# Kernel optimization log

Measured on AMD Instinct MI355X. Metric: run time of the kernel, lower is better.

## Reference

```python
import jax, jax.numpy as jnp
import numpy as np

B, S, D, H = 2, 2048, 2048, 16
DH = D // H
FF = 4 * D
EPS = 1e-5


def setup_inputs() -> dict:
    key = jax.random.key(0)
    ks = jax.random.split(key, 8)
    sd = 0.02
    return {
        "hidden_states": jax.random.normal(ks[0], (B, S, D), jnp.float32),
        "ln1_w": jnp.ones((D,), jnp.float32),
        "ln1_b": jnp.zeros((D,), jnp.float32),
        "qkv_w": jax.random.normal(ks[1], (3 * D, D), jnp.float32) * sd,
        "qkv_b": jnp.zeros((3 * D,), jnp.float32),
        "dense_w": jax.random.normal(ks[2], (D, D), jnp.float32) * sd,
        "dense_b": jnp.zeros((D,), jnp.float32),
        "ln2_w": jnp.ones((D,), jnp.float32),
        "ln2_b": jnp.zeros((D,), jnp.float32),
        "fc1_w": jax.random.normal(ks[3], (FF, D), jnp.float32) * sd,
        "fc1_b": jnp.zeros((FF,), jnp.float32),
        "fc2_w": jax.random.normal(ks[4], (D, FF), jnp.float32) * sd,
        "fc2_b": jnp.zeros((D,), jnp.float32),
    }


def _layer_norm(x, w, b):
    mu = jnp.mean(x, axis=-1, keepdims=True)
    var = jnp.mean(jnp.square(x - mu), axis=-1, keepdims=True)
    return (x - mu) * jax.lax.rsqrt(var + EPS) * w + b


def _attention(x, qkv_w, qkv_b, dense_w, dense_b):
    qkv = x @ qkv_w.T + qkv_b  # [B,S,3D]
    q, k, v = jnp.split(qkv, 3, axis=-1)
    q = q.reshape(B, S, H, DH)
    k = k.reshape(B, S, H, DH)
    v = v.reshape(B, S, H, DH)
    scale = DH ** -0.5
    scores = jnp.einsum("bqhd,bkhd->bhqk", q, k) * scale
    causal = jnp.tril(jnp.ones((S, S), bool))
    scores = jnp.where(causal, scores, jnp.finfo(scores.dtype).min)
    probs = jax.nn.softmax(scores, axis=-1)
    out = jnp.einsum("bhqk,bkhd->bqhd", probs, v).reshape(B, S, D)
    return out @ dense_w.T + dense_b


def reference(hidden_states, ln1_w, ln1_b, qkv_w, qkv_b, dense_w, dense_b,
              ln2_w, ln2_b, fc1_w, fc1_b, fc2_w, fc2_b):
    residual = hidden_states
    x = _layer_norm(hidden_states, ln1_w, ln1_b)
    x = _attention(x, qkv_w, qkv_b, dense_w, dense_b) + residual
    residual = x
    h = _layer_norm(x, ln2_w, ln2_b)
    h = jax.nn.gelu(h @ fc1_w.T + fc1_b, approximate=False)
    h = h @ fc2_w.T + fc2_b
    return residual + h
```

## Files before the change

kernel.cpp:

```cpp
#include <hip/hip_runtime.h>
#include <hip/hip_bf16.h>

#define SEQ    2048
#define DMODEL 2048
#define NHEAD  16
#define DHEAD  128
#define TOK    4096
#define TD     6144
#define FFDIM  8192

typedef __attribute__((ext_vector_type(4)))  float f32x4;
typedef __attribute__((ext_vector_type(16))) float f32x16;
typedef __attribute__((ext_vector_type(8)))  short short8v;

__device__ __forceinline__ void async_ld16(const void* src, void* lds) {
  __builtin_amdgcn_global_load_lds((const __attribute__((address_space(1))) void*)src,
                                   (__attribute__((address_space(3))) void*)lds, 16, 0, 0);
}

__device__ __forceinline__ unsigned pk2(float a, float b) {
  union { __hip_bfloat16 h[2]; unsigned u; } p;
  p.h[0] = __float2bfloat16(a);
  p.h[1] = __float2bfloat16(b);
  return p.u;
}

__global__ __launch_bounds__(256) void f2bf_kernel(const float* __restrict__ in,
                                                   __hip_bfloat16* __restrict__ out, long n) {
  long i0 = ((long)blockIdx.x * 256 + threadIdx.x) * 8;
  long stride = (long)gridDim.x * 256 * 8;
  for (long i = i0; i < n; i += stride) {
    float4 a = *(const float4*)(in + i);
    float4 b = *(const float4*)(in + i + 4);
    union { __hip_bfloat16 h[8]; int4 v; } p;
    p.h[0] = __float2bfloat16(a.x); p.h[1] = __float2bfloat16(a.y);
    p.h[2] = __float2bfloat16(a.z); p.h[3] = __float2bfloat16(a.w);
    p.h[4] = __float2bfloat16(b.x); p.h[5] = __float2bfloat16(b.y);
    p.h[6] = __float2bfloat16(b.z); p.h[7] = __float2bfloat16(b.w);
    *(int4*)(out + i) = p.v;
  }
}

__global__ __launch_bounds__(256) void ln_kernel(const float* __restrict__ x,
                                                 const float* __restrict__ w,
                                                 const float* __restrict__ b,
                                                 __hip_bfloat16* __restrict__ out) {
  __shared__ float red[8];
  const int row = blockIdx.x;
  const int tid = threadIdx.x;
  const float* xr = x + (long)row * DMODEL;
  float4 v0 = ((const float4*)xr)[tid * 2];
  float4 v1 = ((const float4*)xr)[tid * 2 + 1];
  float s  = v0.x + v0.y + v0.z + v0.w + v1.x + v1.y + v1.z + v1.w;
  float ss = v0.x*v0.x + v0.y*v0.y + v0.z*v0.z + v0.w*v0.w
           + v1.x*v1.x + v1.y*v1.y + v1.z*v1.z + v1.w*v1.w;
  #pragma unroll
  for (int m = 1; m < 64; m <<= 1) { s += __shfl_xor(s, m, 64); ss += __shfl_xor(ss, m, 64); }
  if ((tid & 63) == 0) { red[tid >> 6] = s; red[4 + (tid >> 6)] = ss; }
  __syncthreads();
  s  = red[0] + red[1] + red[2] + red[3];
  ss = red[4] + red[5] + red[6] + red[7];
  const float mu = s * (1.0f / DMODEL);
  const float rs = rsqrtf(ss * (1.0f / DMODEL) - mu * mu + 1e-5f);
  float4 w0 = ((const float4*)w)[tid * 2], w1 = ((const float4*)w)[tid * 2 + 1];
  float4 b0 = ((const float4*)b)[tid * 2], b1 = ((const float4*)b)[tid * 2 + 1];
  union { __hip_bfloat16 h[8]; int4 v; } p;
  p.h[0] = __float2bfloat16((v0.x - mu) * rs * w0.x + b0.x);
  p.h[1] = __float2bfloat16((v0.y - mu) * rs * w0.y + b0.y);
  p.h[2] = __float2bfloat16((v0.z - mu) * rs * w0.z + b0.z);
  p.h[3] = __float2bfloat16((v0.w - mu) * rs * w0.w + b0.w);
  p.h[4] = __float2bfloat16((v1.x - mu) * rs * w1.x + b1.x);
  p.h[5] = __float2bfloat16((v1.y - mu) * rs * w1.y + b1.y);
  p.h[6] = __float2bfloat16((v1.z - mu) * rs * w1.z + b1.z);
  p.h[7] = __float2bfloat16((v1.w - mu) * rs * w1.w + b1.w);
  ((int4*)(out + (long)row * DMODEL))[tid] = p.v;
}

template <int MODE, int BM>
__global__ __launch_bounds__(512, 2) void gemm8p(const __hip_bfloat16* __restrict__ A,
                                                 const __hip_bfloat16* __restrict__ B,
                                                 const float* __restrict__ bias,
                                                 const float* __restrict__ resid,
                                                 void* __restrict__ outp,
                                                 int N, long K) {
  constexpr int MR     = BM / 32;
  constexpr int MH     = MR / 2;
  constexpr int A_ISS  = BM / 128;
  constexpr int ABYTES = BM * 64;
  constexpr int BUFB   = ABYTES + 16384;
  __shared__ __align__(16) char lds[4 * BUFB];

  const int tid  = threadIdx.x;
  const int lane = tid & 63;
  const int w    = tid >> 6;
  const int wr   = w >> 2, wc = w & 3;
  const long m0  = (long)blockIdx.y * BM;
  const long n0  = (long)blockIdx.x * 256;
  const int  NT  = (int)(K >> 5);

  const int srow = w * 16 + (lane >> 2);
  const int schk = lane & 3;

  auto stageA = [&](int t) {
    char* base = lds + (t & 3) * BUFB;
    #pragma unroll
    for (int i = 0; i < A_ISS; ++i) {
      int row = srow + i * 128;
      long gc = (long)t * 32 + (long)((schk ^ (row & 3)) * 8);
      async_ld16(A + (m0 + row) * K + gc, base + i * 8192 + w * 1024);
    }
  };
  auto stageB = [&](int t) {
    char* base = lds + (t & 3) * BUFB + ABYTES;
    #pragma unroll
    for (int i = 0; i < 2; ++i) {
      int row = srow + i * 128;
      long gc = (long)t * 32 + (long)((schk ^ (row & 3)) * 8);
      async_ld16(B + (n0 + row) * K + gc, base + i * 8192 + w * 1024);
    }
  };

  f32x4 acc[MR][4] = {};

  #pragma unroll
  for (int t = 0; t < 4; ++t) { stageA(t); stageB(t); }
  if constexpr (BM == 256) asm volatile("s_waitcnt vmcnt(8)\ns_barrier" ::: "memory");
  else                     asm volatile("s_waitcnt vmcnt(6)\ns_barrier" ::: "memory");

  const int c16 = lane >> 4;
  const int l15 = lane & 15;

  for (int t = 0; t < NT; ++t) {
    const int st = (t + 3 < NT) ? t + 3 : NT - 1;
    const char* bb = lds + (t & 3) * BUFB;

    stageA(st);
    short8v bfr[4], af[MH];
    #pragma unroll
    for (int n = 0; n < 4; ++n) {
      int row = wc * 64 + n * 16 + l15;
      bfr[n] = *(const short8v*)(bb + ABYTES + row * 64 + ((c16 ^ (row & 3)) << 4));
    }
    #pragma unroll
    for (int m = 0; m < MH; ++m) {
      int row = wr * (BM / 2) + m * 16 + l15;
      af[m] = *(const short8v*)(bb + row * 64 + ((c16 ^ (row & 3)) << 4));
    }
    __builtin_amdgcn_s_setprio(1);
    #pragma unroll
    for (int m = 0; m < MH; ++m)
      #pragma unroll
      for (int n = 0; n < 4; ++n)
        acc[m][n] = __builtin_amdgcn_mfma_f32_16x16x32_bf16(af[m], bfr[n], acc[m][n], 0, 0, 0);
    __builtin_amdgcn_s_setprio(0);

    stageB(st);
    #pragma unroll
    for (int m = 0; m < MH; ++m) {
      int row = wr * (BM / 2) + (MH + m) * 16 + l15;
      af[m] = *(const short8v*)(bb + row * 64 + ((c16 ^ (row & 3)) << 4));
    }
    __builtin_amdgcn_s_setprio(1);
    #pragma unroll
    for (int m = 0; m < MH; ++m)
      #pragma unroll
      for (int n = 0; n < 4; ++n)
        acc[MH + m][n] = __builtin_amdgcn_mfma_f32_16x16x32_bf16(af[m], bfr[n], acc[MH + m][n], 0, 0, 0);
    __builtin_amdgcn_s_setprio(0);

    if constexpr (BM == 256) asm volatile("s_waitcnt vmcnt(8)\ns_barrier" ::: "memory");
    else                     asm volatile("s_waitcnt vmcnt(6)\ns_barrier" ::: "memory");
  }

  const int colq = l15;
  const int rowq = (lane >> 4) * 4;
  #pragma unroll
  for (int n = 0; n < 4; ++n) {
    long col = n0 + wc * 64 + n * 16 + colq;
    float bi = bias[col];
    #pragma unroll
    for (int mi = 0; mi < MR; ++mi) {
      long row0 = m0 + wr * (BM / 2) + mi * 16 + rowq;
      #pragma unroll
      for (int j = 0; j < 4; ++j) {
        long idx = (row0 + j) * (long)N + col;
        float v = acc[mi][n][j] + bi;
        if (MODE == 0) {
          ((__hip_bfloat16*)outp)[idx] = __float2bfloat16(v);
        } else if (MODE == 1) {
          ((float*)outp)[idx] = v + resid[idx];
        } else {
          float g = 0.5f * v * (1.0f + erff(v * 0.70710678118654752f));
          ((__hip_bfloat16*)outp)[idx] = __float2bfloat16(g);
        }
      }
    }
  }
}

#define QBLK 128
#define KVB  64
#define VSTR 144
#define KBYT 16384
#define VBYT (DHEAD * VSTR)
__global__ __launch_bounds__(256, 2) void attn_kernel(const __hip_bfloat16* __restrict__ qkv,
                                                      __hip_bfloat16* __restrict__ out) {
  __shared__ __align__(16) char smem[2 * KBYT + 2 * VBYT];
  const int tid = threadIdx.x, lane = tid & 63, wid = tid >> 6;
  const int l31 = lane & 31, hi = lane >> 5;
  const int qb = (int)gridDim.x - 1 - (int)blockIdx.x;
  const int q0 = qb * QBLK;
  const int bh = blockIdx.y;
  const int bb = bh >> 4, h = bh & 15;
  const long rowbase = (long)bb * SEQ;
  const int qcol = h * DHEAD, kcol = DMODEL + h * DHEAD, vcol = 2 * DMODEL + h * DHEAD;
  const int qw0 = q0 + wid * 32;

  short8v qf[8];
  {
    const __hip_bfloat16* qp = qkv + (rowbase + qw0 + l31) * TD + qcol + hi * 8;
    #pragma unroll
    for (int kc = 0; kc < 8; ++kc) qf[kc] = *(const short8v*)(qp + kc * 16);
  }

  f32x16 o[4] = {};
  float m_ = -1e30f, l_ = 0.0f;

  const int nt = (q0 + QBLK) / KVB;

  const int kv0s = (tid >> 4) * 4;
  const int dh0s = (tid & 15) * 8;
  auto k_stage = [&](int t) {
    char* kb = smem + (t & 1) * KBYT;
    const long kvr = rowbase + (long)t * KVB;
    #pragma unroll
    for (int i = 0; i < 4; ++i) {
      int c = i * 256 + tid;
      int row = c >> 4, slot = c & 15;
      const void* src = qkv + (kvr + row) * TD + kcol + ((slot ^ (row & 7)) << 3);
      async_ld16(src, kb + i * 4096 + wid * 1024);
    }
  };
  auto v_load = [&](int t, int4* r) {
    const long kvr = rowbase + (long)t * KVB;
    #pragma unroll
    for (int i = 0; i < 4; ++i)
      r[i] = *(const int4*)(qkv + (kvr + kv0s + i) * TD + vcol + dh0s);
  };
  auto v_write = [&](int t, const int4* r) {
    char* vt = smem + 2 * KBYT + (t & 1) * VBYT;
    union { int4 v; unsigned short s[8]; } u0, u1, u2, u3;
    u0.v = r[0]; u1.v = r[1]; u2.v = r[2]; u3.v = r[3];
    #pragma unroll
    for (int dd = 0; dd < 8; ++dd) {
      int d = (dd + ((tid >> 1) & 7)) & 7;
      unsigned lo = (unsigned)u0.s[d] | ((unsigned)u1.s[d] << 16);
      unsigned hi2 = (unsigned)u2.s[d] | ((unsigned)u3.s[d] << 16);
      uint2 wv; wv.x = lo; wv.y = hi2;
      *(uint2*)(vt + (dh0s + d) * VSTR + kv0s * 2) = wv;
    }
  };

  {
    int4 vr[4];
    v_load(0, vr);
    k_stage(0);
    v_write(0, vr);
  }
  __syncthreads();

  for (int t = 0; t < nt; ++t) {
    int4 vr[4];
    const bool more = (t + 1 < nt);
    if (more) { v_load(t + 1, vr); k_stage(t + 1); }

    const int kv0 = t * KVB;
    if (kv0 <= qw0 + 31) {
      const char* Kb = smem + (t & 1) * KBYT;
      f32x16 s0 = {}, s1 = {};
      #pragma unroll
      for (int kc = 0; kc < 8; ++kc) {
        const int colb = kc * 32 + hi * 16;
        const int r0 = l31, r1 = 32 + l31;
        short8v k0 = *(const short8v*)(Kb + r0 * 256 + (colb ^ ((r0 & 7) << 4)));
        short8v k1 = *(const short8v*)(Kb + r1 * 256 + (colb ^ ((r0 & 7) << 4)));
        s0 = __builtin_amdgcn_mfma_f32_32x32x16_bf16(k0, qf[kc], s0, 0, 0, 0);
        s1 = __builtin_amdgcn_mfma_f32_32x32x16_bf16(k1, qf[kc], s1, 0, 0, 0);
      }
      const float scale = 0.08838834764831845f;
      float sv[32];
      #pragma unroll
      for (int r = 0; r < 16; ++r) { sv[r] = s0[r] * scale; sv[16 + r] = s1[r] * scale; }
      const int qg = qw0 + l31;
      if (kv0 + KVB - 1 > qw0) {
        #pragma unroll
        for (int r = 0; r < 16; ++r) {
          int kvr_ = kv0 + (r & 3) + 8 * (r >> 2) + 4 * hi;
          if (kvr_ > qg)      sv[r]      = -1e30f;
          if (kvr_ + 32 > qg) sv[16 + r] = -1e30f;
        }
      }
      float pmax = sv[0];
      #pragma unroll
      for (int r = 1; r < 32; ++r) pmax = fmaxf(pmax, sv[r]);
      pmax = fmaxf(pmax, __shfl_xor(pmax, 32, 64));
      float mn = fmaxf(m_, pmax);
      float alpha = __expf(m_ - mn);
      m_ = mn;
      l_ *= alpha;
      #pragma unroll
      for (int d = 0; d < 4; ++d)
        #pragma unroll
        for (int r = 0; r < 16; ++r) o[d][r] *= alpha;
      float rsum = 0.0f;
      #pragma unroll
      for (int r = 0; r < 32; ++r) { sv[r] = __expf(sv[r] - m_); rsum += sv[r]; }
      l_ += rsum + __shfl_xor(rsum, 32, 64);
      int pa_[4][4];
      #pragma unroll
      for (int kc = 0; kc < 4; ++kc) {
        int ba = 16 * (kc >> 1) + 8 * (kc & 1);
        unsigned wA0 = pk2(sv[ba + 0], sv[ba + 1]);
        unsigned wA1 = pk2(sv[ba + 2], sv[ba + 3]);
        unsigned wB0 = pk2(sv[ba + 4], sv[ba + 5]);
        unsigned wB1 = pk2(sv[ba + 6], sv[ba + 7]);
        unsigned z0 = (unsigned)__shfl_xor((int)(hi ? wA0 : wB0), 32, 64);
        unsigned z1 = (unsigned)__shfl_xor((int)(hi ? wA1 : wB1), 32, 64);
        pa_[kc][0] = hi ? (int)z0 : (int)wA0;
        pa_[kc][1] = hi ? (int)z1 : (int)wA1;
        pa_[kc][2] = hi ? (int)wB0 : (int)z0;
        pa_[kc][3] = hi ? (int)wB1 : (int)z1;
      }
      const char* Vt = smem + 2 * KBYT + (t & 1) * VBYT;
      #pragma unroll
      for (int dht = 0; dht < 4; ++dht) {
        const int dh = dht * 32 + l31;
        short8v vf[4];
        #pragma unroll
        for (int kc = 0; kc < 4; ++kc)
          vf[kc] = *(const short8v*)(Vt + dh * VSTR + kc * 32 + hi * 16);
        #pragma unroll
        for (int kc = 0; kc < 4; ++kc) {
          union { int i[4]; short8v v; } bv;
          bv.i[0] = pa_[kc][0]; bv.i[1] = pa_[kc][1];
          bv.i[2] = pa_[kc][2]; bv.i[3] = pa_[kc][3];
          o[dht] = __builtin_amdgcn_mfma_f32_32x32x16_bf16(vf[kc], bv.v, o[dht], 0, 0, 0);
        }
      }
    }
    if (more) v_write(t + 1, vr);
    __syncthreads();
  }

  const float linv = 1.0f / l_;
  const long orow = (rowbase + qw0 + l31) * DMODEL + h * DHEAD;
  #pragma unroll
  for (int dht = 0; dht < 4; ++dht)
    #pragma unroll
    for (int rg = 0; rg < 4; ++rg) {
      union { __hip_bfloat16 hh[4]; uint2 u; } pk;
      #pragma unroll
      for (int i = 0; i < 4; ++i) pk.hh[i] = __float2bfloat16(o[dht][rg * 4 + i] * linv);
      *(uint2*)(out + orow + dht * 32 + 8 * rg + 4 * hi) = pk.u;
    }
}

extern "C" void kernel_launch(void* const* d_in, const int* in_sizes, int n_in,
                              void* d_out, int out_size, void* d_ws, size_t ws_size,
                              hipStream_t stream) {
  const float* hidden  = (const float*)d_in[0];
  const float* ln1w    = (const float*)d_in[1];
  const float* ln1b    = (const float*)d_in[2];
  const float* qkvw    = (const float*)d_in[3];
  const float* qkvb    = (const float*)d_in[4];
  const float* densew  = (const float*)d_in[5];
  const float* denseb  = (const float*)d_in[6];
  const float* ln2w    = (const float*)d_in[7];
  const float* ln2b    = (const float*)d_in[8];
  const float* fc1w    = (const float*)d_in[9];
  const float* fc1b    = (const float*)d_in[10];
  const float* fc2w    = (const float*)d_in[11];
  const float* fc2b    = (const float*)d_in[12];

  char* ws = (char*)d_ws;
  size_t off = 0;
  auto alloc = [&](size_t bytes) { char* p = ws + off; off += (bytes + 255) & ~(size_t)255; return p; };
  __hip_bfloat16* xbf    = (__hip_bfloat16*)alloc((size_t)TOK * DMODEL * 2);
  __hip_bfloat16* wqkv   = (__hip_bfloat16*)alloc((size_t)TD * DMODEL * 2);
  __hip_bfloat16* wdense = (__hip_bfloat16*)alloc((size_t)DMODEL * DMODEL * 2);
  __hip_bfloat16* wfc1   = (__hip_bfloat16*)alloc((size_t)FFDIM * DMODEL * 2);
  __hip_bfloat16* wfc2   = (__hip_bfloat16*)alloc((size_t)DMODEL * FFDIM * 2);
  __hip_bfloat16* big    = (__hip_bfloat16*)alloc((size_t)TOK * FFDIM * 2);
  float*          x2     = (float*)alloc((size_t)TOK * DMODEL * 4);
  __hip_bfloat16* qkvbuf  = big;
  __hip_bfloat16* attnout = big + (size_t)TOK * TD;
  __hip_bfloat16* gelubuf = big;

  f2bf_kernel<<<1024, 256, 0, stream>>>(qkvw,   wqkv,   (long)TD * DMODEL);
  f2bf_kernel<<<1024, 256, 0, stream>>>(densew, wdense, (long)DMODEL * DMODEL);
  f2bf_kernel<<<1024, 256, 0, stream>>>(fc1w,   wfc1,   (long)FFDIM * DMODEL);
  f2bf_kernel<<<1024, 256, 0, stream>>>(fc2w,   wfc2,   (long)DMODEL * FFDIM);

  ln_kernel<<<TOK, 256, 0, stream>>>(hidden, ln1w, ln1b, xbf);
  gemm8p<0, 256><<<dim3(TD / 256, TOK / 256), 512, 0, stream>>>(xbf, wqkv, qkvb, nullptr, qkvbuf, TD, DMODEL);
  attn_kernel<<<dim3(SEQ / QBLK, 2 * NHEAD), 256, 0, stream>>>(qkvbuf, attnout);
  gemm8p<1, 128><<<dim3(DMODEL / 256, TOK / 128), 512, 0, stream>>>(attnout, wdense, denseb, hidden, x2, DMODEL, DMODEL);
  ln_kernel<<<TOK, 256, 0, stream>>>(x2, ln2w, ln2b, xbf);
  gemm8p<2, 256><<<dim3(FFDIM / 256, TOK / 256), 512, 0, stream>>>(xbf, wfc1, fc1b, nullptr, gelubuf, FFDIM, DMODEL);
  gemm8p<1, 128><<<dim3(DMODEL / 256, TOK / 128), 512, 0, stream>>>(gelubuf, wfc2, fc2b, x2, (float*)d_out, DMODEL, FFDIM);
}
```

Before: 744.0 us.

## Replace pipelined GEMM with simple 128x128 tiled GEMM and pair attention query blocks

Swaps the four-stage async-pipelined 256-wide GEMM for a single-buffered 128x128 tile GEMM with 256 threads, 64-wide K steps, an XOR-swizzled LDS layout and an XCD-aware block swizzle. The attention kernel now processes two query blocks per workgroup (one from each end of the causal range) to balance work under the causal mask, halving the grid. The GEMM loses software pipelining and the larger-tile reuse, so loads and MFMA work are no longer overlapped within a block.

```diff
diff --git a/kernel.cpp b/kernel.cpp
--- a/kernel.cpp
+++ b/kernel.cpp
@@ -76,115 +76,81 @@
   ((int4*)(out + (long)row * DMODEL))[tid] = p.v;
 }
 
-template <int MODE, int BM>
-__global__ __launch_bounds__(512, 2) void gemm8p(const __hip_bfloat16* __restrict__ A,
-                                                 const __hip_bfloat16* __restrict__ B,
-                                                 const float* __restrict__ bias,
-                                                 const float* __restrict__ resid,
-                                                 void* __restrict__ outp,
-                                                 int N, long K) {
-  constexpr int MR     = BM / 32;
-  constexpr int MH     = MR / 2;
-  constexpr int A_ISS  = BM / 128;
-  constexpr int ABYTES = BM * 64;
-  constexpr int BUFB   = ABYTES + 16384;
-  __shared__ __align__(16) char lds[4 * BUFB];
-
-  const int tid  = threadIdx.x;
+template <int MODE>
+__global__ __launch_bounds__(256) void gemm_bt(const __hip_bfloat16* __restrict__ A,
+                                               const __hip_bfloat16* __restrict__ B,
+                                               const float* __restrict__ bias,
+                                               const float* __restrict__ resid,
+                                               void* __restrict__ outp,
+                                               int N, long K) {
+  __shared__ __align__(16) char lds[32768];
+  const int tid = threadIdx.x;
   const int lane = tid & 63;
-  const int w    = tid >> 6;
-  const int wr   = w >> 2, wc = w & 3;
-  const long m0  = (long)blockIdx.y * BM;
-  const long n0  = (long)blockIdx.x * 256;
-  const int  NT  = (int)(K >> 5);
-
-  const int srow = w * 16 + (lane >> 2);
-  const int schk = lane & 3;
-
-  auto stageA = [&](int t) {
-    char* base = lds + (t & 3) * BUFB;
-    #pragma unroll
-    for (int i = 0; i < A_ISS; ++i) {
-      int row = srow + i * 128;
-      long gc = (long)t * 32 + (long)((schk ^ (row & 3)) * 8);
-      async_ld16(A + (m0 + row) * K + gc, base + i * 8192 + w * 1024);
-    }
-  };
-  auto stageB = [&](int t) {
-    char* base = lds + (t & 3) * BUFB + ABYTES;
-    #pragma unroll
-    for (int i = 0; i < 2; ++i) {
-      int row = srow + i * 128;
-      long gc = (long)t * 32 + (long)((schk ^ (row & 3)) * 8);
-      async_ld16(B + (n0 + row) * K + gc, base + i * 8192 + w * 1024);
-    }
-  };
-
-  f32x4 acc[MR][4] = {};
-
-  #pragma unroll
-  for (int t = 0; t < 4; ++t) { stageA(t); stageB(t); }
-  if constexpr (BM == 256) asm volatile("s_waitcnt vmcnt(8)\ns_barrier" ::: "memory");
-  else                     asm volatile("s_waitcnt vmcnt(6)\ns_barrier" ::: "memory");
-
-  const int c16 = lane >> 4;
-  const int l15 = lane & 15;
-
-  for (int t = 0; t < NT; ++t) {
-    const int st = (t + 3 < NT) ? t + 3 : NT - 1;
-    const char* bb = lds + (t & 3) * BUFB;
-
-    stageA(st);
-    short8v bfr[4], af[MH];
-    #pragma unroll
-    for (int n = 0; n < 4; ++n) {
-      int row = wc * 64 + n * 16 + l15;
-      bfr[n] = *(const short8v*)(bb + ABYTES + row * 64 + ((c16 ^ (row & 3)) << 4));
-    }
-    #pragma unroll
-    for (int m = 0; m < MH; ++m) {
-      int row = wr * (BM / 2) + m * 16 + l15;
-      af[m] = *(const short8v*)(bb + row * 64 + ((c16 ^ (row & 3)) << 4));
-    }
-    __builtin_amdgcn_s_setprio(1);
-    #pragma unroll
-    for (int m = 0; m < MH; ++m)
-      #pragma unroll
-      for (int n = 0; n < 4; ++n)
-        acc[m][n] = __builtin_amdgcn_mfma_f32_16x16x32_bf16(af[m], bfr[n], acc[m][n], 0, 0, 0);
-    __builtin_amdgcn_s_setprio(0);
-
-    stageB(st);
-    #pragma unroll
-    for (int m = 0; m < MH; ++m) {
-      int row = wr * (BM / 2) + (MH + m) * 16 + l15;
-      af[m] = *(const short8v*)(bb + row * 64 + ((c16 ^ (row & 3)) << 4));
-    }
-    __builtin_amdgcn_s_setprio(1);
-    #pragma unroll
-    for (int m = 0; m < MH; ++m)
-      #pragma unroll
-      for (int n = 0; n < 4; ++n)
-        acc[MH + m][n] = __builtin_amdgcn_mfma_f32_16x16x32_bf16(af[m], bfr[n], acc[MH + m][n], 0, 0, 0);
-    __builtin_amdgcn_s_setprio(0);
-
-    if constexpr (BM == 256) asm volatile("s_waitcnt vmcnt(8)\ns_barrier" ::: "memory");
-    else                     asm volatile("s_waitcnt vmcnt(6)\ns_barrier" ::: "memory");
+  const int wid = tid >> 6;
+  const int wr = wid >> 1, wc = wid & 1;
+  const int gx = gridDim.x;
+  const int nwg = gx * (int)gridDim.y;
+  const int lin = (int)blockIdx.y * gx + (int)blockIdx.x;
+  const int cpx = nwg >> 3;
+  const int swz = (lin & 7) * cpx + (lin >> 3);
+  const long m0 = (long)(swz / gx) * 128;
+  const long n0 = (long)(swz % gx) * 128;
+
+  const int lrow = lane >> 3;
+  const long ksrc = (long)(((lane & 7) ^ lrow) * 8);
+
+  f32x4 acc[4][4] = {};
+
+  for (long kt = 0; kt < K; kt += 64) {
+    __syncthreads();
+    #pragma unroll
+    for (int c = 0; c < 8; ++c) {
+      int region = wid * 8 + c;
+      int isB = region >> 4;
+      int rr = region & 15;
+      int row = rr * 8 + lrow;
+      const __hip_bfloat16* srcbase = isB ? B : A;
+      long grow = (isB ? n0 : m0) + row;
+      const __hip_bfloat16* src = srcbase + grow * K + kt + ksrc;
+      async_ld16(src, lds + isB * 16384 + rr * 1024);
+    }
+    __syncthreads();
+    #pragma unroll
+    for (int kk = 0; kk < 2; ++kk) {
+      short8v af[4], bfr[4];
+      #pragma unroll
+      for (int m = 0; m < 4; ++m) {
+        int row = wr * 64 + m * 16 + (lane & 15);
+        int kb = kk * 64 + (lane >> 4) * 16;
+        af[m] = *(const short8v*)(lds + row * 128 + (kb ^ ((row & 7) << 4)));
+      }
+      #pragma unroll
+      for (int n = 0; n < 4; ++n) {
+        int row = wc * 64 + n * 16 + (lane & 15);
+        int kb = kk * 64 + (lane >> 4) * 16;
+        bfr[n] = *(const short8v*)(lds + 16384 + row * 128 + (kb ^ ((row & 7) << 4)));
+      }
+      #pragma unroll
+      for (int m = 0; m < 4; ++m)
+        #pragma unroll
+        for (int n = 0; n < 4; ++n)
+          acc[m][n] = __builtin_amdgcn_mfma_f32_16x16x32_bf16(af[m], bfr[n], acc[m][n], 0, 0, 0);
+    }
   }
 
-  const int colq = l15;
+  const int colq = lane & 15;
   const int rowq = (lane >> 4) * 4;
   #pragma unroll
   for (int n = 0; n < 4; ++n) {
     long col = n0 + wc * 64 + n * 16 + colq;
     float bi = bias[col];
     #pragma unroll
-    for (int mi = 0; mi < MR; ++mi) {
-      long row0 = m0 + wr * (BM / 2) + mi * 16 + rowq;
+    for (int m = 0; m < 4; ++m) {
+      long row0 = m0 + wr * 64 + m * 16 + rowq;
       #pragma unroll
       for (int j = 0; j < 4; ++j) {
         long idx = (row0 + j) * (long)N + col;
-        float v = acc[mi][n][j] + bi;
+        float v = acc[m][n][j] + bi;
         if (MODE == 0) {
           ((__hip_bfloat16*)outp)[idx] = __float2bfloat16(v);
         } else if (MODE == 1) {
@@ -208,25 +174,11 @@
   __shared__ __align__(16) char smem[2 * KBYT + 2 * VBYT];
   const int tid = threadIdx.x, lane = tid & 63, wid = tid >> 6;
   const int l31 = lane & 31, hi = lane >> 5;
-  const int qb = (int)gridDim.x - 1 - (int)blockIdx.x;
-  const int q0 = qb * QBLK;
+  const int bx = blockIdx.x;
   const int bh = blockIdx.y;
   const int bb = bh >> 4, h = bh & 15;
   const long rowbase = (long)bb * SEQ;
   const int qcol = h * DHEAD, kcol = DMODEL + h * DHEAD, vcol = 2 * DMODEL + h * DHEAD;
-  const int qw0 = q0 + wid * 32;
-
-  short8v qf[8];
-  {
-    const __hip_bfloat16* qp = qkv + (rowbase + qw0 + l31) * TD + qcol + hi * 8;
-    #pragma unroll
-    for (int kc = 0; kc < 8; ++kc) qf[kc] = *(const short8v*)(qp + kc * 16);
-  }
-
-  f32x16 o[4] = {};
-  float m_ = -1e30f, l_ = 0.0f;
-
-  const int nt = (q0 + QBLK) / KVB;
 
   const int kv0s = (tid >> 4) * 4;
   const int dh0s = (tid & 15) * 8;
@@ -261,108 +213,126 @@
     }
   };
 
-  {
-    int4 vr[4];
-    v_load(0, vr);
-    k_stage(0);
-    v_write(0, vr);
+  #pragma unroll
+  for (int mem = 0; mem < 2; ++mem) {
+    const int qb = mem == 0 ? (15 - bx) : bx;
+    const int q0 = qb * QBLK;
+    const int qw0 = q0 + wid * 32;
+
+    short8v qf[8];
+    {
+      const __hip_bfloat16* qp = qkv + (rowbase + qw0 + l31) * TD + qcol + hi * 8;
+      #pragma unroll
+      for (int kc = 0; kc < 8; ++kc) qf[kc] = *(const short8v*)(qp + kc * 16);
+    }
+
+    f32x16 o[4] = {};
+    float m_ = -1e30f, l_ = 0.0f;
+    const int nt = (q0 + QBLK) / KVB;
+
+    {
+      int4 vr[4];
+      v_load(0, vr);
+      k_stage(0);
+      v_write(0, vr);
+    }
+    __syncthreads();
+
+    for (int t = 0; t < nt; ++t) {
+      int4 vr[4];
+      const bool more = (t + 1 < nt);
+      if (more) { v_load(t + 1, vr); k_stage(t + 1); }
+
+      const int kv0 = t * KVB;
+      if (kv0 <= qw0 + 31) {
+        const char* Kb = smem + (t & 1) * KBYT;
+        f32x16 s0 = {}, s1 = {};
+        #pragma unroll
+        for (int kc = 0; kc < 8; ++kc) {
+          const int colb = kc * 32 + hi * 16;
+          const int r0 = l31, r1 = 32 + l31;
+          short8v k0 = *(const short8v*)(Kb + r0 * 256 + (colb ^ ((r0 & 7) << 4)));
+          short8v k1 = *(const short8v*)(Kb + r1 * 256 + (colb ^ ((r0 & 7) << 4)));
+          s0 = __builtin_amdgcn_mfma_f32_32x32x16_bf16(k0, qf[kc], s0, 0, 0, 0);
+          s1 = __builtin_amdgcn_mfma_f32_32x32x16_bf16(k1, qf[kc], s1, 0, 0, 0);
+        }
+        const float scale = 0.08838834764831845f;
+        float sv[32];
+        #pragma unroll
+        for (int r = 0; r < 16; ++r) { sv[r] = s0[r] * scale; sv[16 + r] = s1[r] * scale; }
+        const int qg = qw0 + l31;
+        if (kv0 + KVB - 1 > qw0) {
+          #pragma unroll
+          for (int r = 0; r < 16; ++r) {
+            int kvr_ = kv0 + (r & 3) + 8 * (r >> 2) + 4 * hi;
+            if (kvr_ > qg)      sv[r]      = -1e30f;
+            if (kvr_ + 32 > qg) sv[16 + r] = -1e30f;
+          }
+        }
+        float pmax = sv[0];
+        #pragma unroll
+        for (int r = 1; r < 32; ++r) pmax = fmaxf(pmax, sv[r]);
+        pmax = fmaxf(pmax, __shfl_xor(pmax, 32, 64));
+        float mn = fmaxf(m_, pmax);
+        float alpha = __expf(m_ - mn);
+        m_ = mn;
+        l_ *= alpha;
+        #pragma unroll
+        for (int d = 0; d < 4; ++d)
+          #pragma unroll
+          for (int r = 0; r < 16; ++r) o[d][r] *= alpha;
+        float rsum = 0.0f;
+        #pragma unroll
+        for (int r = 0; r < 32; ++r) { sv[r] = __expf(sv[r] - m_); rsum += sv[r]; }
+        l_ += rsum + __shfl_xor(rsum, 32, 64);
+        int pa_[4][4];
+        #pragma unroll
+        for (int kc = 0; kc < 4; ++kc) {
+          int ba = 16 * (kc >> 1) + 8 * (kc & 1);
+          unsigned wA0 = pk2(sv[ba + 0], sv[ba + 1]);
+          unsigned wA1 = pk2(sv[ba + 2], sv[ba + 3]);
+          unsigned wB0 = pk2(sv[ba + 4], sv[ba + 5]);
+          unsigned wB1 = pk2(sv[ba + 6], sv[ba + 7]);
+          unsigned z0 = (unsigned)__shfl_xor((int)(hi ? wA0 : wB0), 32, 64);
+          unsigned z1 = (unsigned)__shfl_xor((int)(hi ? wA1 : wB1), 32, 64);
+          pa_[kc][0] = hi ? (int)z0 : (int)wA0;
+          pa_[kc][1] = hi ? (int)z1 : (int)wA1;
+          pa_[kc][2] = hi ? (int)wB0 : (int)z0;
+          pa_[kc][3] = hi ? (int)wB1 : (int)z1;
+        }
+        const char* Vt = smem + 2 * KBYT + (t & 1) * VBYT;
+        #pragma unroll
+        for (int dht = 0; dht < 4; ++dht) {
+          const int dh = dht * 32 + l31;
+          short8v vf[4];
+          #pragma unroll
+          for (int kc = 0; kc < 4; ++kc)
+            vf[kc] = *(const short8v*)(Vt + dh * VSTR + kc * 32 + hi * 16);
+          #pragma unroll
+          for (int kc = 0; kc < 4; ++kc) {
+            union { int i[4]; short8v v; } bv;
+            bv.i[0] = pa_[kc][0]; bv.i[1] = pa_[kc][1];
+            bv.i[2] = pa_[kc][2]; bv.i[3] = pa_[kc][3];
+            o[dht] = __builtin_amdgcn_mfma_f32_32x32x16_bf16(vf[kc], bv.v, o[dht], 0, 0, 0);
+          }
+        }
+      }
+      if (more) v_write(t + 1, vr);
+      __syncthreads();
+    }
+
+    const float linv = 1.0f / l_;
+    const long orow = (rowbase + qw0 + l31) * DMODEL + h * DHEAD;
+    #pragma unroll
+    for (int dht = 0; dht < 4; ++dht)
+      #pragma unroll
+      for (int rg = 0; rg < 4; ++rg) {
+        union { __hip_bfloat16 hh[4]; uint2 u; } pk;
+        #pragma unroll
+        for (int i = 0; i < 4; ++i) pk.hh[i] = __float2bfloat16(o[dht][rg * 4 + i] * linv);
+        *(uint2*)(out + orow + dht * 32 + 8 * rg + 4 * hi) = pk.u;
+      }
   }
-  __syncthreads();
-
-  for (int t = 0; t < nt; ++t) {
-    int4 vr[4];
-    const bool more = (t + 1 < nt);
-    if (more) { v_load(t + 1, vr); k_stage(t + 1); }
-
-    const int kv0 = t * KVB;
-    if (kv0 <= qw0 + 31) {
-      const char* Kb = smem + (t & 1) * KBYT;
-      f32x16 s0 = {}, s1 = {};
-      #pragma unroll
-      for (int kc = 0; kc < 8; ++kc) {
-        const int colb = kc * 32 + hi * 16;
-        const int r0 = l31, r1 = 32 + l31;
-        short8v k0 = *(const short8v*)(Kb + r0 * 256 + (colb ^ ((r0 & 7) << 4)));
-        short8v k1 = *(const short8v*)(Kb + r1 * 256 + (colb ^ ((r0 & 7) << 4)));
-        s0 = __builtin_amdgcn_mfma_f32_32x32x16_bf16(k0, qf[kc], s0, 0, 0, 0);
-        s1 = __builtin_amdgcn_mfma_f32_32x32x16_bf16(k1, qf[kc], s1, 0, 0, 0);
-      }
-      const float scale = 0.08838834764831845f;
-      float sv[32];
-      #pragma unroll
-      for (int r = 0; r < 16; ++r) { sv[r] = s0[r] * scale; sv[16 + r] = s1[r] * scale; }
-      const int qg = qw0 + l31;
-      if (kv0 + KVB - 1 > qw0) {
-        #pragma unroll
-        for (int r = 0; r < 16; ++r) {
-          int kvr_ = kv0 + (r & 3) + 8 * (r >> 2) + 4 * hi;
-          if (kvr_ > qg)      sv[r]      = -1e30f;
-          if (kvr_ + 32 > qg) sv[16 + r] = -1e30f;
-        }
-      }
-      float pmax = sv[0];
-      #pragma unroll
-      for (int r = 1; r < 32; ++r) pmax = fmaxf(pmax, sv[r]);
-      pmax = fmaxf(pmax, __shfl_xor(pmax, 32, 64));
-      float mn = fmaxf(m_, pmax);
-      float alpha = __expf(m_ - mn);
-      m_ = mn;
-      l_ *= alpha;
-      #pragma unroll
-      for (int d = 0; d < 4; ++d)
-        #pragma unroll
-        for (int r = 0; r < 16; ++r) o[d][r] *= alpha;
-      float rsum = 0.0f;
-      #pragma unroll
-      for (int r = 0; r < 32; ++r) { sv[r] = __expf(sv[r] - m_); rsum += sv[r]; }
-      l_ += rsum + __shfl_xor(rsum, 32, 64);
-      int pa_[4][4];
-      #pragma unroll
-      for (int kc = 0; kc < 4; ++kc) {
-        int ba = 16 * (kc >> 1) + 8 * (kc & 1);
-        unsigned wA0 = pk2(sv[ba + 0], sv[ba + 1]);
-        unsigned wA1 = pk2(sv[ba + 2], sv[ba + 3]);
-        unsigned wB0 = pk2(sv[ba + 4], sv[ba + 5]);
-        unsigned wB1 = pk2(sv[ba + 6], sv[ba + 7]);
-        unsigned z0 = (unsigned)__shfl_xor((int)(hi ? wA0 : wB0), 32, 64);
-        unsigned z1 = (unsigned)__shfl_xor((int)(hi ? wA1 : wB1), 32, 64);
-        pa_[kc][0] = hi ? (int)z0 : (int)wA0;
-        pa_[kc][1] = hi ? (int)z1 : (int)wA1;
-        pa_[kc][2] = hi ? (int)wB0 : (int)z0;
-        pa_[kc][3] = hi ? (int)wB1 : (int)z1;
-      }
-      const char* Vt = smem + 2 * KBYT + (t & 1) * VBYT;
-      #pragma unroll
-      for (int dht = 0; dht < 4; ++dht) {
-        const int dh = dht * 32 + l31;
-        short8v vf[4];
-        #pragma unroll
-        for (int kc = 0; kc < 4; ++kc)
-          vf[kc] = *(const short8v*)(Vt + dh * VSTR + kc * 32 + hi * 16);
-        #pragma unroll
-        for (int kc = 0; kc < 4; ++kc) {
-          union { int i[4]; short8v v; } bv;
-          bv.i[0] = pa_[kc][0]; bv.i[1] = pa_[kc][1];
-          bv.i[2] = pa_[kc][2]; bv.i[3] = pa_[kc][3];
-          o[dht] = __builtin_amdgcn_mfma_f32_32x32x16_bf16(vf[kc], bv.v, o[dht], 0, 0, 0);
-        }
-      }
-    }
-    if (more) v_write(t + 1, vr);
-    __syncthreads();
-  }
-
-  const float linv = 1.0f / l_;
-  const long orow = (rowbase + qw0 + l31) * DMODEL + h * DHEAD;
-  #pragma unroll
-  for (int dht = 0; dht < 4; ++dht)
-    #pragma unroll
-    for (int rg = 0; rg < 4; ++rg) {
-      union { __hip_bfloat16 hh[4]; uint2 u; } pk;
-      #pragma unroll
-      for (int i = 0; i < 4; ++i) pk.hh[i] = __float2bfloat16(o[dht][rg * 4 + i] * linv);
-      *(uint2*)(out + orow + dht * 32 + 8 * rg + 4 * hi) = pk.u;
-    }
 }
 
 extern "C" void kernel_launch(void* const* d_in, const int* in_sizes, int n_in,
@@ -402,10 +372,10 @@
   f2bf_kernel<<<1024, 256, 0, stream>>>(fc2w,   wfc2,   (long)DMODEL * FFDIM);
 
   ln_kernel<<<TOK, 256, 0, stream>>>(hidden, ln1w, ln1b, xbf);
-  gemm8p<0, 256><<<dim3(TD / 256, TOK / 256), 512, 0, stream>>>(xbf, wqkv, qkvb, nullptr, qkvbuf, TD, DMODEL);
-  attn_kernel<<<dim3(SEQ / QBLK, 2 * NHEAD), 256, 0, stream>>>(qkvbuf, attnout);
-  gemm8p<1, 128><<<dim3(DMODEL / 256, TOK / 128), 512, 0, stream>>>(attnout, wdense, denseb, hidden, x2, DMODEL, DMODEL);
+  gemm_bt<0><<<dim3(TD / 128, TOK / 128), 256, 0, stream>>>(xbf, wqkv, qkvb, nullptr, qkvbuf, TD, DMODEL);
+  attn_kernel<<<dim3(8, 2 * NHEAD), 256, 0, stream>>>(qkvbuf, attnout);
+  gemm_bt<1><<<dim3(DMODEL / 128, TOK / 128), 256, 0, stream>>>(attnout, wdense, denseb, hidden, x2, DMODEL, DMODEL);
   ln_kernel<<<TOK, 256, 0, stream>>>(x2, ln2w, ln2b, xbf);
-  gemm8p<2, 256><<<dim3(FFDIM / 256, TOK / 256), 512, 0, stream>>>(xbf, wfc1, fc1b, nullptr, gelubuf, FFDIM, DMODEL);
-  gemm8p<1, 128><<<dim3(DMODEL / 256, TOK / 128), 512, 0, stream>>>(gelubuf, wfc2, fc2b, x2, (float*)d_out, DMODEL, FFDIM);
-}
+  gemm_bt<2><<<dim3(FFDIM / 128, TOK / 128), 256, 0, stream>>>(xbf, wfc1, fc1b, nullptr, gelubuf, FFDIM, DMODEL);
+  gemm_bt<1><<<dim3(DMODEL / 128, TOK / 128), 256, 0, stream>>>(gelubuf, wfc2, fc2b, x2, (float*)d_out, DMODEL, FFDIM);
+}
```

After: 795.9 us. 7.0% more time.
